# Optimization experiments

Measured on AMD Instinct MI355X. Metric: run time of the kernel, lower is better.

## Reference

```python
import jax, jax.numpy as jnp
import numpy as np

# Faithful JAX translation of fastmax_function with mask=True, p=1, normalize=0.
# In that branch the torch code sets temperature = 1 and uses a0 = a1 = 1.

def setup_inputs() -> dict:
    key = jax.random.key(0)
    kq, kk, kv = jax.random.split(key, 3)
    b, h, n, d = 2, 8, 8192, 32
    q = jax.random.normal(kq, (b, h, n, d), dtype=jnp.float32)
    k = jax.random.normal(kk, (b, h, n, d), dtype=jnp.float32)
    v = jax.random.normal(kv, (b, h, n, d), dtype=jnp.float32)
    return {"q": q, "k": k, "v": v}


def reference(q, k, v):
    # q, k, v: (b, h, n, d); causal (mask=True), p=1, a0=a1=1, temperature=1
    b, h, n, d = q.shape
    # first term: running sum of values
    first = jnp.cumsum(v, axis=2)                                  # (b,h,n,d)
    # second term: q_i . (sum_{j<=i} k_j v_j^T)
    kv = jnp.einsum('bhnd,bhne->bhnde', k, v)                      # (b,h,n,d,d)
    kv_cs = jnp.cumsum(kv, axis=2)                                 # (b,h,n,d,d)
    second = jnp.einsum('bhnd,bhnde->bhne', q, kv_cs)              # (b,h,n,d)
    # denominator: i + q_i . (sum_{j<=i} k_j)
    k_cs = jnp.cumsum(k, axis=2)                                   # (b,h,n,d)
    div1 = jnp.arange(1, n + 1, dtype=q.dtype)                     # (n,)
    div2 = jnp.einsum('bhnd,bhnd->bhn', q, k_cs)                   # (b,h,n)
    div = (div1[None, None, :] + div2)[..., None]                  # (b,h,n,1)
    return (first + second) / div
```

## Files before the change

### kernel.cpp

```cpp
#include <hip/hip_runtime.h>


#define D      32
#define C      64
#define NCHUNK 128
#define GSIZE  4
#define NGROUP 32
#define BH     16
#define NBLK   (BH * NCHUNK)
#define NGRP   (NBLK / GSIZE)
#define AGGU   1152

typedef __attribute__((ext_vector_type(8))) short bf16x8;
typedef __attribute__((ext_vector_type(4))) float f32x4;
typedef __attribute__((ext_vector_type(4))) unsigned short u16x4;

__device__ __forceinline__ unsigned short f2bf(float x) {
  union { float f; unsigned u; } c; c.f = x;
  unsigned r = (c.u + 0x7FFFu + ((c.u >> 16) & 1u)) >> 16;
  return (unsigned short)r;
}
__device__ __forceinline__ float bf2f(unsigned short u) {
  union { unsigned u; float f; } c; c.u = ((unsigned)u) << 16;
  return c.f;
}
__device__ __forceinline__ int permcol(int e) {
  return (e & 1) ? (16 + (e >> 1)) : (e >> 1);
}

__global__ __launch_bounds__(256) void state_scan_kernel(
    const float* __restrict__ k, const float* __restrict__ v,
    unsigned short* __restrict__ pref, unsigned short* __restrict__ gtot) {
  __shared__ __align__(16) unsigned short kT[D * 72];
  __shared__ __align__(16) unsigned short vT[D * 72];
  __shared__ __align__(16) float psK[1024];
  __shared__ __align__(16) float psV[1024];

  int t  = threadIdx.x;
  int j0 = t >> 3;
  int cb = (t & 7) * 4;
  int lane = t & 63, w = t >> 6;
  int m16 = lane & 15, quad = lane >> 4;
  int mb = w >> 1, nb = w & 1;
  int d1b = 16 * mb + quad * 4;
  int np  = permcol(16 * nb + m16);

  int c0 = blockIdx.x * GSIZE;
  const float4* kp = (const float4*)k + (size_t)c0 * 512;
  const float4* vp = (const float4*)v + (size_t)c0 * 512;

  float pr[4] = {0.f, 0.f, 0.f, 0.f};
  float tailpref = 0.f;

  float4 kA = kp[t], kB = kp[t + 256];
  float4 vA = vp[t], vB = vp[t + 256];

  for (int ci = 0; ci < GSIZE; ++ci) {
    {
      const float* ka = &kA.x; const float* kb = &kB.x;
      const float* va = &vA.x; const float* vb = &vB.x;
#pragma unroll
      for (int cc = 0; cc < 4; ++cc) {
        kT[(cb + cc) * 72 + j0]      = f2bf(ka[cc]);
        kT[(cb + cc) * 72 + j0 + 32] = f2bf(kb[cc]);
        vT[(cb + cc) * 72 + j0]      = f2bf(va[cc]);
        vT[(cb + cc) * 72 + j0 + 32] = f2bf(vb[cc]);
      }
      *(float4*)&psK[4 * t] =
          make_float4(kA.x + kB.x, kA.y + kB.y, kA.z + kB.z, kA.w + kB.w);
      *(float4*)&psV[4 * t] =
          make_float4(vA.x + vB.x, vA.y + vB.y, vA.z + vB.z, vA.w + vB.w);
    }
    __syncthreads();

    if (ci + 1 < GSIZE) {
      const float4* kn = kp + (size_t)(ci + 1) * 512;
      const float4* vn = vp + (size_t)(ci + 1) * 512;
      kA = kn[t]; kB = kn[t + 256];
      vA = vn[t]; vB = vn[t + 256];
    }

    f32x4 acc = {0.f, 0.f, 0.f, 0.f};
#pragma unroll
    for (int kb2 = 0; kb2 < 2; ++kb2) {
      bf16x8 a = *(const bf16x8*)&kT[(16 * mb + m16) * 72 + kb2 * 32 + quad * 8];
      bf16x8 b = *(const bf16x8*)&vT[(16 * nb + m16) * 72 + kb2 * 32 + quad * 8];
      acc = __builtin_amdgcn_mfma_f32_16x16x32_bf16(a, b, acc, 0, 0, 0);
    }
    float csum = 0.f;
    if (t < 64) {
      int ee = t & 31;
      const float* ps = (t < 32) ? psK : psV;
#pragma unroll
      for (int m = 0; m < 32; ++m) csum += ps[ee + 32 * m];
    }

    unsigned short* pc = pref + (size_t)(c0 + ci) * AGGU;
    *(u16x4*)&pc[np * 32 + d1b] =
        (u16x4){f2bf(pr[0]), f2bf(pr[1]), f2bf(pr[2]), f2bf(pr[3])};
#pragma unroll
    for (int reg = 0; reg < 4; ++reg) pr[reg] += acc[reg];
    if (t < 64) {
      ((float*)(pc + 1024))[t] = tailpref;
      tailpref += csum;
    }
    __syncthreads();
  }

  unsigned short* gt = gtot + (size_t)blockIdx.x * AGGU;
  *(u16x4*)&gt[np * 32 + d1b] =
      (u16x4){f2bf(pr[0]), f2bf(pr[1]), f2bf(pr[2]), f2bf(pr[3])};
  if (t < 64) ((float*)(gt + 1024))[t] = tailpref;
}

__global__ __launch_bounds__(256, 4) void output_kernel(
    const float* __restrict__ q, const float* __restrict__ k,
    const float* __restrict__ v, const unsigned short* __restrict__ pref,
    const unsigned short* __restrict__ gtot, float* __restrict__ out) {
  int blk = blockIdx.x;
  int c   = blk & 127;
  int bh  = blk >> 7;
  int g   = c >> 2;
  size_t off = (size_t)blk * (C * D);
  const float4* qp4 = (const float4*)q + (size_t)blk * 512;
  const float4* kp4 = (const float4*)k + (size_t)blk * 512;
  const float4* vp4 = (const float4*)v + (size_t)blk * 512;
  const unsigned short* prf = pref + (size_t)blk * AGGU;
  const unsigned short* gtb = gtot + (size_t)(bh * NGROUP) * AGGU;

  __shared__ __align__(16) char uA[10240];
  unsigned short* qbf = (unsigned short*)uA;
  unsigned short* kbf = (unsigned short*)(uA + 5120);
  float* q_s = (float*)uA;
  __shared__ __align__(16) unsigned short vTbf[D * 72];
  __shared__ __align__(16) unsigned short kvTbf[D * 40];
  __shared__ __align__(16) unsigned short Tbf[C * 72];
  __shared__ __align__(16) float kc_s[C * 36];
  __shared__ __align__(16) float gtot_s[8 * 32];
  __shared__ __align__(16) float pre_s[64];
  __shared__ __align__(16) float invdiv_s[C];

  int t  = threadIdx.x;
  int j0 = t >> 3;
  int cb = (t & 7) * 4;

  float4 qA = qp4[t], qB = qp4[t + 256];
  float4 kA = kp4[t], kB = kp4[t + 256];
  float4 vA = vp4[t], vB = vp4[t + 256];

  uint2 rp = *(const uint2*)&prf[4 * t];
  float tlp = 0.f;
  if (t < 64) tlp = ((const float*)(prf + 1024))[t];
  float s0 = bf2f((unsigned short)(rp.x & 0xffff));
  float s1 = bf2f((unsigned short)(rp.x >> 16));
  float s2 = bf2f((unsigned short)(rp.y & 0xffff));
  float s3 = bf2f((unsigned short)(rp.y >> 16));
  float tf = tlp;
  for (int p0 = 0; p0 < g; p0 += 8) {
    uint2 r[8]; float tl[8];
#pragma unroll
    for (int u = 0; u < 8; ++u) {
      int p = p0 + u;
      const unsigned short* gp = gtb + (size_t)(p < g ? p : 0) * AGGU;
      r[u] = *(const uint2*)&gp[4 * t];
      if (t < 64) tl[u] = ((const float*)(gp + 1024))[t];
    }
#pragma unroll
    for (int u = 0; u < 8; ++u) {
      if (p0 + u < g) {
        s0 += bf2f((unsigned short)(r[u].x & 0xffff));
        s1 += bf2f((unsigned short)(r[u].x >> 16));
        s2 += bf2f((unsigned short)(r[u].y & 0xffff));
        s3 += bf2f((unsigned short)(r[u].y >> 16));
        if (t < 64) tf += tl[u];
      }
    }
  }

  for (int z = t; z < (C * 72) / 8; z += 256)
    ((uint4*)Tbf)[z] = make_uint4(0, 0, 0, 0);

  *(float4*)&kc_s[j0 * 36 + cb]        = kA;
  *(float4*)&kc_s[(j0 + 32) * 36 + cb] = kB;
  *(u16x4*)&qbf[j0 * 40 + cb] =
      (u16x4){f2bf(qA.x), f2bf(qA.y), f2bf(qA.z), f2bf(qA.w)};
  *(u16x4*)&qbf[(j0 + 32) * 40 + cb] =
      (u16x4){f2bf(qB.x), f2bf(qB.y), f2bf(qB.z), f2bf(qB.w)};
  *(u16x4*)&kbf[j0 * 40 + cb] =
      (u16x4){f2bf(kA.x), f2bf(kA.y), f2bf(kA.z), f2bf(kA.w)};
  *(u16x4*)&kbf[(j0 + 32) * 40 + cb] =
      (u16x4){f2bf(kB.x), f2bf(kB.y), f2bf(kB.z), f2bf(kB.w)};
  {
    const float* va = &vA.x; const float* vb = &vB.x;
#pragma unroll
    for (int cc = 0; cc < 4; ++cc) {
      int n = permcol(cb + cc);
      vTbf[n * 72 + j0]      = f2bf(va[cc]);
      vTbf[n * 72 + j0 + 32] = f2bf(vb[cc]);
    }
  }
  *(u16x4*)&kvTbf[(t >> 3) * 40 + (t & 7) * 4] =
      (u16x4){f2bf(s0), f2bf(s1), f2bf(s2), f2bf(s3)};
  if (t < 64) pre_s[t] = tf;
  __syncthreads();

  int lane = t & 63, w = t >> 6;
  int m16 = lane & 15, quad = lane >> 4;

  const bf16x8 aQ = *(const bf16x8*)&qbf[(16 * w + m16) * 40 + quad * 8];
  for (int jb = 0; jb <= w; ++jb) {
    bf16x8 bK = *(const bf16x8*)&kbf[(16 * jb + m16) * 40 + quad * 8];
    f32x4 cS = {0.f, 0.f, 0.f, 0.f};
    cS = __builtin_amdgcn_mfma_f32_16x16x32_bf16(aQ, bK, cS, 0, 0, 0);
    int jcol = 16 * jb + m16;
#pragma unroll
    for (int reg = 0; reg < 4; ++reg) {
      int i = 16 * w + quad * 4 + reg;
      float tv = (jcol <= i) ? (1.f + cS[reg]) : 0.f;
      Tbf[i * 72 + jcol] = f2bf(tv);
    }
  }
  int rg = t >> 5;
  int e  = t & 31;
  float vals[8];
  {
    float run = 0.f;
#pragma unroll
    for (int r = 0; r < 8; ++r) {
      vals[r] = kc_s[(rg * 8 + r) * 36 + e];
      run += vals[r];
    }
    gtot_s[rg * 32 + e] = run;
  }
  __syncthreads();

  {
    float offv = pre_s[e];
    for (int g2 = 0; g2 < rg; ++g2) offv += gtot_s[g2 * 32 + e];
    float cacc = offv;
#pragma unroll
    for (int r = 0; r < 8; ++r) {
      cacc += vals[r];
      kc_s[(rg * 8 + r) * 36 + e] = cacc;
    }
  }
  *(float4*)&q_s[j0 * 36 + cb]        = qA;
  *(float4*)&q_s[(j0 + 32) * 36 + cb] = qB;
  __syncthreads();

  if (t < 64) {
    int i = t;
    float dp = 0.f;
#pragma unroll
    for (int d4 = 0; d4 < 8; ++d4) {
      float4 qv = *(const float4*)&q_s[i * 36 + 4 * d4];
      float4 kc = *(const float4*)&kc_s[i * 36 + 4 * d4];
      dp += qv.x * kc.x + qv.y * kc.y + qv.z * kc.z + qv.w * kc.w;
    }
    invdiv_s[i] = 1.f / ((float)(c * C + i + 1) + dp);
  }
  f32x4 o0 = {0.f, 0.f, 0.f, 0.f}, o1 = {0.f, 0.f, 0.f, 0.f};
  {
    bf16x8 b0 = *(const bf16x8*)&kvTbf[(m16)      * 40 + quad * 8];
    bf16x8 b1 = *(const bf16x8*)&kvTbf[(16 + m16) * 40 + quad * 8];
    o0 = __builtin_amdgcn_mfma_f32_16x16x32_bf16(aQ, b0, o0, 0, 0, 0);
    o1 = __builtin_amdgcn_mfma_f32_16x16x32_bf16(aQ, b1, o1, 0, 0, 0);
  }
  int kbcnt = (w >= 2) ? 2 : 1;
  for (int kb2 = 0; kb2 < kbcnt; ++kb2) {
    bf16x8 aT = *(const bf16x8*)&Tbf[(16 * w + m16) * 72 + kb2 * 32 + quad * 8];
    bf16x8 b0 = *(const bf16x8*)&vTbf[(m16)      * 72 + kb2 * 32 + quad * 8];
    bf16x8 b1 = *(const bf16x8*)&vTbf[(16 + m16) * 72 + kb2 * 32 + quad * 8];
    o0 = __builtin_amdgcn_mfma_f32_16x16x32_bf16(aT, b0, o0, 0, 0, 0);
    o1 = __builtin_amdgcn_mfma_f32_16x16x32_bf16(aT, b1, o1, 0, 0, 0);
  }
  __syncthreads();

  int e0 = 2 * m16;
#pragma unroll
  for (int reg = 0; reg < 4; ++reg) {
    int i = 16 * w + quad * 4 + reg;
    float id = invdiv_s[i];
    float2 o;
    o.x = (pre_s[32 + e0]     + o0[reg]) * id;
    o.y = (pre_s[32 + e0 + 1] + o1[reg]) * id;
    *(float2*)&out[off + (size_t)i * D + e0] = o;
  }
}

extern "C" void kernel_launch(void* const* d_in, const int* in_sizes, int n_in,
                              void* d_out, int out_size, void* d_ws, size_t ws_size,
                              hipStream_t stream) {
  const float* q = (const float*)d_in[0];
  const float* k = (const float*)d_in[1];
  const float* v = (const float*)d_in[2];
  float* out = (float*)d_out;
  unsigned short* pref = (unsigned short*)d_ws;
  unsigned short* gtot = pref + (size_t)NBLK * AGGU;

  state_scan_kernel<<<NGRP, 256, 0, stream>>>(k, v, pref, gtot);
  output_kernel<<<NBLK, 256, 0, stream>>>(q, k, v, pref, gtot, out);
}
```

Measured before the change: 106.2 us.

## Process four chunks per output block with shared group prefix and prefetch

The output kernel now launches one block per group of four chunks instead of one per chunk. The group-level prefix sum over earlier groups is computed once and reused across the four chunks, and the next chunk's q/k/v and prefix data are prefetched into registers while the current chunk computes. This removes redundant prefix reads and overlaps global loads with compute. In exchange the grid shrinks from 2048 to 512 blocks, which lowers parallelism and adds extra barriers and register pressure.

Result: faster. 103.6 us, median of 2 (-2.5%).

```diff
diff --git a/kernel.cpp b/kernel.cpp
--- a/kernel.cpp
+++ b/kernel.cpp
@@ -117,15 +117,13 @@
     const float* __restrict__ q, const float* __restrict__ k,
     const float* __restrict__ v, const unsigned short* __restrict__ pref,
     const unsigned short* __restrict__ gtot, float* __restrict__ out) {
-  int blk = blockIdx.x;
-  int c   = blk & 127;
-  int bh  = blk >> 7;
-  int g   = c >> 2;
-  size_t off = (size_t)blk * (C * D);
-  const float4* qp4 = (const float4*)q + (size_t)blk * 512;
-  const float4* kp4 = (const float4*)k + (size_t)blk * 512;
-  const float4* vp4 = (const float4*)v + (size_t)blk * 512;
-  const unsigned short* prf = pref + (size_t)blk * AGGU;
+  int g   = blockIdx.x & 31;
+  int bh  = blockIdx.x >> 5;
+  int blk0 = blockIdx.x * GSIZE;
+  const float4* qp4 = (const float4*)q + (size_t)blk0 * 512;
+  const float4* kp4 = (const float4*)k + (size_t)blk0 * 512;
+  const float4* vp4 = (const float4*)v + (size_t)blk0 * 512;
+  const unsigned short* prf = pref + (size_t)blk0 * AGGU;
   const unsigned short* gtb = gtot + (size_t)(bh * NGROUP) * AGGU;
 
   __shared__ __align__(16) char uA[10240];
@@ -143,19 +141,12 @@
   int t  = threadIdx.x;
   int j0 = t >> 3;
   int cb = (t & 7) * 4;
-
-  float4 qA = qp4[t], qB = qp4[t + 256];
-  float4 kA = kp4[t], kB = kp4[t + 256];
-  float4 vA = vp4[t], vB = vp4[t + 256];
-
-  uint2 rp = *(const uint2*)&prf[4 * t];
-  float tlp = 0.f;
-  if (t < 64) tlp = ((const float*)(prf + 1024))[t];
-  float s0 = bf2f((unsigned short)(rp.x & 0xffff));
-  float s1 = bf2f((unsigned short)(rp.x >> 16));
-  float s2 = bf2f((unsigned short)(rp.y & 0xffff));
-  float s3 = bf2f((unsigned short)(rp.y >> 16));
-  float tf = tlp;
+  int lane = t & 63, w = t >> 6;
+  int m16 = lane & 15, quad = lane >> 4;
+  int rg = t >> 5;
+  int e  = t & 31;
+
+  float gs0 = 0.f, gs1 = 0.f, gs2 = 0.f, gs3 = 0.f, gtf = 0.f;
   for (int p0 = 0; p0 < g; p0 += 8) {
     uint2 r[8]; float tl[8];
 #pragma unroll
@@ -168,123 +159,157 @@
 #pragma unroll
     for (int u = 0; u < 8; ++u) {
       if (p0 + u < g) {
-        s0 += bf2f((unsigned short)(r[u].x & 0xffff));
-        s1 += bf2f((unsigned short)(r[u].x >> 16));
-        s2 += bf2f((unsigned short)(r[u].y & 0xffff));
-        s3 += bf2f((unsigned short)(r[u].y >> 16));
-        if (t < 64) tf += tl[u];
+        gs0 += bf2f((unsigned short)(r[u].x & 0xffff));
+        gs1 += bf2f((unsigned short)(r[u].x >> 16));
+        gs2 += bf2f((unsigned short)(r[u].y & 0xffff));
+        gs3 += bf2f((unsigned short)(r[u].y >> 16));
+        if (t < 64) gtf += tl[u];
       }
     }
   }
 
-  for (int z = t; z < (C * 72) / 8; z += 256)
-    ((uint4*)Tbf)[z] = make_uint4(0, 0, 0, 0);
-
-  *(float4*)&kc_s[j0 * 36 + cb]        = kA;
-  *(float4*)&kc_s[(j0 + 32) * 36 + cb] = kB;
-  *(u16x4*)&qbf[j0 * 40 + cb] =
-      (u16x4){f2bf(qA.x), f2bf(qA.y), f2bf(qA.z), f2bf(qA.w)};
-  *(u16x4*)&qbf[(j0 + 32) * 40 + cb] =
-      (u16x4){f2bf(qB.x), f2bf(qB.y), f2bf(qB.z), f2bf(qB.w)};
-  *(u16x4*)&kbf[j0 * 40 + cb] =
-      (u16x4){f2bf(kA.x), f2bf(kA.y), f2bf(kA.z), f2bf(kA.w)};
-  *(u16x4*)&kbf[(j0 + 32) * 40 + cb] =
-      (u16x4){f2bf(kB.x), f2bf(kB.y), f2bf(kB.z), f2bf(kB.w)};
-  {
-    const float* va = &vA.x; const float* vb = &vB.x;
-#pragma unroll
-    for (int cc = 0; cc < 4; ++cc) {
-      int n = permcol(cb + cc);
-      vTbf[n * 72 + j0]      = f2bf(va[cc]);
-      vTbf[n * 72 + j0 + 32] = f2bf(vb[cc]);
-    }
-  }
-  *(u16x4*)&kvTbf[(t >> 3) * 40 + (t & 7) * 4] =
-      (u16x4){f2bf(s0), f2bf(s1), f2bf(s2), f2bf(s3)};
-  if (t < 64) pre_s[t] = tf;
-  __syncthreads();
-
-  int lane = t & 63, w = t >> 6;
-  int m16 = lane & 15, quad = lane >> 4;
-
-  const bf16x8 aQ = *(const bf16x8*)&qbf[(16 * w + m16) * 40 + quad * 8];
-  for (int jb = 0; jb <= w; ++jb) {
-    bf16x8 bK = *(const bf16x8*)&kbf[(16 * jb + m16) * 40 + quad * 8];
-    f32x4 cS = {0.f, 0.f, 0.f, 0.f};
-    cS = __builtin_amdgcn_mfma_f32_16x16x32_bf16(aQ, bK, cS, 0, 0, 0);
-    int jcol = 16 * jb + m16;
+  float4 qA = qp4[t], qB = qp4[t + 256];
+  float4 kA = kp4[t], kB = kp4[t + 256];
+  float4 vA = vp4[t], vB = vp4[t + 256];
+  uint2 rp = *(const uint2*)&prf[4 * t];
+  float tlp = (t < 64) ? ((const float*)(prf + 1024))[t] : 0.f;
+
+  for (int ci = 0; ci < GSIZE; ++ci) {
+    int blk = blk0 + ci;
+    int c   = blk & 127;
+    size_t off = (size_t)blk * (C * D);
+
+    if (ci == 0) {
+      for (int z = t; z < (C * 72) / 8; z += 256)
+        ((uint4*)Tbf)[z] = make_uint4(0, 0, 0, 0);
+    }
+
+    *(float4*)&kc_s[j0 * 36 + cb]        = kA;
+    *(float4*)&kc_s[(j0 + 32) * 36 + cb] = kB;
+    *(u16x4*)&qbf[j0 * 40 + cb] =
+        (u16x4){f2bf(qA.x), f2bf(qA.y), f2bf(qA.z), f2bf(qA.w)};
+    *(u16x4*)&qbf[(j0 + 32) * 40 + cb] =
+        (u16x4){f2bf(qB.x), f2bf(qB.y), f2bf(qB.z), f2bf(qB.w)};
+    *(u16x4*)&kbf[j0 * 40 + cb] =
+        (u16x4){f2bf(kA.x), f2bf(kA.y), f2bf(kA.z), f2bf(kA.w)};
+    *(u16x4*)&kbf[(j0 + 32) * 40 + cb] =
+        (u16x4){f2bf(kB.x), f2bf(kB.y), f2bf(kB.z), f2bf(kB.w)};
+    {
+      const float* va = &vA.x; const float* vb = &vB.x;
+#pragma unroll
+      for (int cc = 0; cc < 4; ++cc) {
+        int n = permcol(cb + cc);
+        vTbf[n * 72 + j0]      = f2bf(va[cc]);
+        vTbf[n * 72 + j0 + 32] = f2bf(vb[cc]);
+      }
+    }
+    {
+      float s0 = gs0 + bf2f((unsigned short)(rp.x & 0xffff));
+      float s1 = gs1 + bf2f((unsigned short)(rp.x >> 16));
+      float s2 = gs2 + bf2f((unsigned short)(rp.y & 0xffff));
+      float s3 = gs3 + bf2f((unsigned short)(rp.y >> 16));
+      *(u16x4*)&kvTbf[(t >> 3) * 40 + (t & 7) * 4] =
+          (u16x4){f2bf(s0), f2bf(s1), f2bf(s2), f2bf(s3)};
+    }
+    if (t < 64) pre_s[t] = gtf + tlp;
+    __syncthreads();
+
+    float4 nqA = make_float4(0,0,0,0), nqB = nqA, nkA = nqA, nkB = nqA,
+           nvA = nqA, nvB = nqA;
+    uint2 nrp = make_uint2(0, 0); float ntlp = 0.f;
+    if (ci + 1 < GSIZE) {
+      const float4* qn = qp4 + (size_t)(ci + 1) * 512;
+      const float4* kn = kp4 + (size_t)(ci + 1) * 512;
+      const float4* vn = vp4 + (size_t)(ci + 1) * 512;
+      nqA = qn[t]; nqB = qn[t + 256];
+      nkA = kn[t]; nkB = kn[t + 256];
+      nvA = vn[t]; nvB = vn[t + 256];
+      const unsigned short* pn = prf + (size_t)(ci + 1) * AGGU;
+      nrp = *(const uint2*)&pn[4 * t];
+      if (t < 64) ntlp = ((const float*)(pn + 1024))[t];
+    }
+
+    const bf16x8 aQ = *(const bf16x8*)&qbf[(16 * w + m16) * 40 + quad * 8];
+    for (int jb = 0; jb <= w; ++jb) {
+      bf16x8 bK = *(const bf16x8*)&kbf[(16 * jb + m16) * 40 + quad * 8];
+      f32x4 cS = {0.f, 0.f, 0.f, 0.f};
+      cS = __builtin_amdgcn_mfma_f32_16x16x32_bf16(aQ, bK, cS, 0, 0, 0);
+      int jcol = 16 * jb + m16;
+#pragma unroll
+      for (int reg = 0; reg < 4; ++reg) {
+        int i = 16 * w + quad * 4 + reg;
+        float tv = (jcol <= i) ? (1.f + cS[reg]) : 0.f;
+        Tbf[i * 72 + jcol] = f2bf(tv);
+      }
+    }
+    float vals[8];
+    {
+      float run = 0.f;
+#pragma unroll
+      for (int r = 0; r < 8; ++r) {
+        vals[r] = kc_s[(rg * 8 + r) * 36 + e];
+        run += vals[r];
+      }
+      gtot_s[rg * 32 + e] = run;
+    }
+    __syncthreads();
+
+    {
+      float offv = pre_s[e];
+      for (int g2 = 0; g2 < rg; ++g2) offv += gtot_s[g2 * 32 + e];
+      float cacc = offv;
+#pragma unroll
+      for (int r = 0; r < 8; ++r) {
+        cacc += vals[r];
+        kc_s[(rg * 8 + r) * 36 + e] = cacc;
+      }
+    }
+    *(float4*)&q_s[j0 * 36 + cb]        = qA;
+    *(float4*)&q_s[(j0 + 32) * 36 + cb] = qB;
+    __syncthreads();
+
+    if (t < 64) {
+      int i = t;
+      float dp = 0.f;
+#pragma unroll
+      for (int d4 = 0; d4 < 8; ++d4) {
+        float4 qv = *(const float4*)&q_s[i * 36 + 4 * d4];
+        float4 kc = *(const float4*)&kc_s[i * 36 + 4 * d4];
+        dp += qv.x * kc.x + qv.y * kc.y + qv.z * kc.z + qv.w * kc.w;
+      }
+      invdiv_s[i] = 1.f / ((float)(c * C + i + 1) + dp);
+    }
+    f32x4 o0 = {0.f, 0.f, 0.f, 0.f}, o1 = {0.f, 0.f, 0.f, 0.f};
+    {
+      bf16x8 b0 = *(const bf16x8*)&kvTbf[(m16)      * 40 + quad * 8];
+      bf16x8 b1 = *(const bf16x8*)&kvTbf[(16 + m16) * 40 + quad * 8];
+      o0 = __builtin_amdgcn_mfma_f32_16x16x32_bf16(aQ, b0, o0, 0, 0, 0);
+      o1 = __builtin_amdgcn_mfma_f32_16x16x32_bf16(aQ, b1, o1, 0, 0, 0);
+    }
+    int kbcnt = (w >= 2) ? 2 : 1;
+    for (int kb2 = 0; kb2 < kbcnt; ++kb2) {
+      bf16x8 aT = *(const bf16x8*)&Tbf[(16 * w + m16) * 72 + kb2 * 32 + quad * 8];
+      bf16x8 b0 = *(const bf16x8*)&vTbf[(m16)      * 72 + kb2 * 32 + quad * 8];
+      bf16x8 b1 = *(const bf16x8*)&vTbf[(16 + m16) * 72 + kb2 * 32 + quad * 8];
+      o0 = __builtin_amdgcn_mfma_f32_16x16x32_bf16(aT, b0, o0, 0, 0, 0);
+      o1 = __builtin_amdgcn_mfma_f32_16x16x32_bf16(aT, b1, o1, 0, 0, 0);
+    }
+    __syncthreads();
+
+    int e0 = 2 * m16;
 #pragma unroll
     for (int reg = 0; reg < 4; ++reg) {
       int i = 16 * w + quad * 4 + reg;
-      float tv = (jcol <= i) ? (1.f + cS[reg]) : 0.f;
-      Tbf[i * 72 + jcol] = f2bf(tv);
-    }
-  }
-  int rg = t >> 5;
-  int e  = t & 31;
-  float vals[8];
-  {
-    float run = 0.f;
-#pragma unroll
-    for (int r = 0; r < 8; ++r) {
-      vals[r] = kc_s[(rg * 8 + r) * 36 + e];
-      run += vals[r];
-    }
-    gtot_s[rg * 32 + e] = run;
-  }
-  __syncthreads();
-
-  {
-    float offv = pre_s[e];
-    for (int g2 = 0; g2 < rg; ++g2) offv += gtot_s[g2 * 32 + e];
-    float cacc = offv;
-#pragma unroll
-    for (int r = 0; r < 8; ++r) {
-      cacc += vals[r];
-      kc_s[(rg * 8 + r) * 36 + e] = cacc;
-    }
-  }
-  *(float4*)&q_s[j0 * 36 + cb]        = qA;
-  *(float4*)&q_s[(j0 + 32) * 36 + cb] = qB;
-  __syncthreads();
-
-  if (t < 64) {
-    int i = t;
-    float dp = 0.f;
-#pragma unroll
-    for (int d4 = 0; d4 < 8; ++d4) {
-      float4 qv = *(const float4*)&q_s[i * 36 + 4 * d4];
-      float4 kc = *(const float4*)&kc_s[i * 36 + 4 * d4];
-      dp += qv.x * kc.x + qv.y * kc.y + qv.z * kc.z + qv.w * kc.w;
-    }
-    invdiv_s[i] = 1.f / ((float)(c * C + i + 1) + dp);
-  }
-  f32x4 o0 = {0.f, 0.f, 0.f, 0.f}, o1 = {0.f, 0.f, 0.f, 0.f};
-  {
-    bf16x8 b0 = *(const bf16x8*)&kvTbf[(m16)      * 40 + quad * 8];
-    bf16x8 b1 = *(const bf16x8*)&kvTbf[(16 + m16) * 40 + quad * 8];
-    o0 = __builtin_amdgcn_mfma_f32_16x16x32_bf16(aQ, b0, o0, 0, 0, 0);
-    o1 = __builtin_amdgcn_mfma_f32_16x16x32_bf16(aQ, b1, o1, 0, 0, 0);
-  }
-  int kbcnt = (w >= 2) ? 2 : 1;
-  for (int kb2 = 0; kb2 < kbcnt; ++kb2) {
-    bf16x8 aT = *(const bf16x8*)&Tbf[(16 * w + m16) * 72 + kb2 * 32 + quad * 8];
-    bf16x8 b0 = *(const bf16x8*)&vTbf[(m16)      * 72 + kb2 * 32 + quad * 8];
-    bf16x8 b1 = *(const bf16x8*)&vTbf[(16 + m16) * 72 + kb2 * 32 + quad * 8];
-    o0 = __builtin_amdgcn_mfma_f32_16x16x32_bf16(aT, b0, o0, 0, 0, 0);
-    o1 = __builtin_amdgcn_mfma_f32_16x16x32_bf16(aT, b1, o1, 0, 0, 0);
-  }
-  __syncthreads();
-
-  int e0 = 2 * m16;
-#pragma unroll
-  for (int reg = 0; reg < 4; ++reg) {
-    int i = 16 * w + quad * 4 + reg;
-    float id = invdiv_s[i];
-    float2 o;
-    o.x = (pre_s[32 + e0]     + o0[reg]) * id;
-    o.y = (pre_s[32 + e0 + 1] + o1[reg]) * id;
-    *(float2*)&out[off + (size_t)i * D + e0] = o;
+      float id = invdiv_s[i];
+      float2 o;
+      o.x = (pre_s[32 + e0]     + o0[reg]) * id;
+      o.y = (pre_s[32 + e0 + 1] + o1[reg]) * id;
+      *(float2*)&out[off + (size_t)i * D + e0] = o;
+    }
+    __syncthreads();
+
+    qA = nqA; qB = nqB; kA = nkA; kB = nkB; vA = nvA; vB = nvB;
+    rp = nrp; tlp = ntlp;
   }
 }
 
@@ -299,5 +324,5 @@
   unsigned short* gtot = pref + (size_t)NBLK * AGGU;
 
   state_scan_kernel<<<NGRP, 256, 0, stream>>>(k, v, pref, gtot);
-  output_kernel<<<NBLK, 256, 0, stream>>>(q, k, v, pref, gtot, out);
-}
+  output_kernel<<<NGRP, 256, 0, stream>>>(q, k, v, pref, gtot, out);
+}
```
